# Optimization experiments

Measured on AMD Instinct MI355X. Metric: run time of the kernel, lower is better.

The kernel has to match this reference:

```python
import jax, jax.numpy as jnp
import numpy as np

N_NODES = 50000
N_EDGES = 800000
IN_FEAT = 128
NUM_CLASSES = 40


def _glorot(key, shape):
    fan_in, fan_out = shape
    lim = jnp.sqrt(6.0 / (fan_in + fan_out))
    return jax.random.uniform(key, shape, jnp.float32, -lim, lim)


def setup_inputs() -> dict:
    key = jax.random.key(0)
    ks = jax.random.split(key, 16)
    inp = {
        "x": jax.random.normal(ks[0], (N_NODES, IN_FEAT), jnp.float32),
        "edge_index": jax.random.randint(ks[1], (2, N_EDGES), 0, N_NODES, jnp.int64),
        "edge_weight": jax.random.uniform(ks[2], (N_EDGES,), jnp.float32),
        # GCNConv weights (PyG GCNConv: linear w/o bias, separate bias added after aggregation)
        "W1": _glorot(ks[3], (IN_FEAT, 512)), "b1": jnp.zeros((512,), jnp.float32),
        "W2": _glorot(ks[4], (512, 256)), "b2": jnp.zeros((256,), jnp.float32),
        "W3": _glorot(ks[5], (256, 128)), "b3": jnp.zeros((128,), jnp.float32),
        # MLP head
        "L1w": _glorot(ks[6], (128, 64)), "L1b": jnp.zeros((64,), jnp.float32),
        "L2w": _glorot(ks[7], (64, 32)), "L2b": jnp.zeros((32,), jnp.float32),
        "L3w": _glorot(ks[8], (32, NUM_CLASSES)), "L3b": jnp.zeros((NUM_CLASSES,), jnp.float32),
    }
    return inp


def _gcn_conv(x, W, b, src, dst, ew, n):
    # PyG GCNConv: add self-loops (weight 1), symmetric normalization D^-1/2 (A+I) D^-1/2,
    # linear transform first, then scatter-add aggregation, then bias.
    xw = x @ W  # [N, C_out]
    deg = jax.ops.segment_sum(ew, dst, num_segments=n) + 1.0  # +1 for self-loop weight
    dinv = jnp.where(deg > 0, jax.lax.rsqrt(deg), 0.0)  # [N]
    norm = dinv[src] * ew * dinv[dst]  # [E]
    out = jax.ops.segment_sum(norm[:, None] * xw[src], dst, num_segments=n)
    out = out + (dinv * dinv)[:, None] * xw  # self-loop contribution
    return out + b


def reference(x, edge_index, edge_weight, W1, b1, W2, b2, W3, b3,
              L1w, L1b, L2w, L2b, L3w, L3b):
    n = x.shape[0]
    src, dst = edge_index[0], edge_index[1]
    # conv stack; dropout p=0.0 -> identity (omitted)
    h = jax.nn.relu(_gcn_conv(x, W1, b1, src, dst, edge_weight, n))
    h = jax.nn.relu(_gcn_conv(h, W2, b2, src, dst, edge_weight, n))
    h = jax.nn.relu(_gcn_conv(h, W3, b3, src, dst, edge_weight, n))
    # MLP head
    h = jax.nn.relu(h @ L1w + L1b)
    h = jax.nn.relu(h @ L2w + L2b)
    h = h @ L3w + L3b
    return jax.nn.softmax(h, axis=1)
```

## Files before the change

### kernel.cpp

```cpp
#include <hip/hip_runtime.h>
#include <hip/hip_bf16.h>

#define N_NODES 50000
#define N_EDGES 800000
#define M_PAD 50048

typedef __attribute__((ext_vector_type(8))) short short8;
typedef __attribute__((ext_vector_type(4))) float float4_;

#define GLOAD_LDS(g, l) __builtin_amdgcn_global_load_lds( \
    (const __attribute__((address_space(1))) void*)(g),   \
    (__attribute__((address_space(3))) void*)(l), 16, 0, 0)

__device__ __forceinline__ unsigned short f2bf(float f) {
    unsigned int u = __float_as_uint(f);
    unsigned int r = (u + 0x7FFFu + ((u >> 16) & 1u)) >> 16;
    return (unsigned short)r;
}
__device__ __forceinline__ float bf2f(unsigned short h) {
    return __uint_as_float(((unsigned int)h) << 16);
}


__global__ __launch_bounds__(256) void deg_kernel(const int* __restrict__ dst,
                                                  const float* __restrict__ ew,
                                                  float* __restrict__ deg, int E) {
    int e = blockIdx.x * blockDim.x + threadIdx.x;
    if (e < E) atomicAdd(&deg[dst[e]], ew[e]);
}

__global__ __launch_bounds__(256) void dinv_kernel(float* __restrict__ deg, int n) {
    int i = blockIdx.x * blockDim.x + threadIdx.x;
    if (i < n) deg[i] = rsqrtf(deg[i] + 1.0f);
}


__global__ __launch_bounds__(256) void count_kernel(const int* __restrict__ dst,
                                                    int* __restrict__ cnt, int E) {
    int e = blockIdx.x * blockDim.x + threadIdx.x;
    if (e < E) atomicAdd(&cnt[dst[e]], 1);
}

__global__ __launch_bounds__(512) void scan_block_kernel(const int* __restrict__ cnt,
                                                         int* __restrict__ rowptr,
                                                         int* __restrict__ bsums, int n) {
    __shared__ int s[512];
    int t = threadIdx.x;
    int i = blockIdx.x * 512 + t;
    s[t] = (i < n) ? cnt[i] : 0;
    __syncthreads();
    for (int off = 1; off < 512; off <<= 1) {
        int v = (t >= off) ? s[t - off] : 0;
        __syncthreads();
        s[t] += v;
        __syncthreads();
    }
    if (i < n) rowptr[i + 1] = s[t];
    if (t == 511) bsums[blockIdx.x] = s[511];
}

__global__ void scan_sums_kernel(int* bsums, int nb) {
    if (threadIdx.x == 0 && blockIdx.x == 0) {
        int run = 0;
        for (int i = 0; i < nb; ++i) { int v = bsums[i]; bsums[i] = run; run += v; }
    }
}

__global__ __launch_bounds__(512) void scan_add_kernel(int* __restrict__ rowptr,
                                                       const int* __restrict__ bsums, int n) {
    int i = blockIdx.x * 512 + threadIdx.x;
    if (i < n) rowptr[i + 1] += bsums[blockIdx.x];
    if (i == 0) rowptr[0] = 0;
}

__global__ __launch_bounds__(256) void fill_kernel(const int* __restrict__ src,
                                                   const int* __restrict__ dst,
                                                   const float* __restrict__ ew,
                                                   const float* __restrict__ dinv,
                                                   int* __restrict__ cursor,
                                                   int* __restrict__ col,
                                                   float* __restrict__ val, int E) {
    int e = blockIdx.x * blockDim.x + threadIdx.x;
    if (e >= E) return;
    int d = dst[e];
    int s = src[e];
    int pos = atomicAdd(&cursor[d], 1);
    col[pos] = s;
    val[pos] = dinv[s] * ew[e];
}


__global__ __launch_bounds__(256) void wsplit_kernel(const float* __restrict__ Wm,
                                                     unsigned short* __restrict__ Th,
                                                     unsigned short* __restrict__ Tl,
                                                     int K, int N) {
    int idx = blockIdx.x * blockDim.x + threadIdx.x;
    if (idx >= K * N) return;
    int n = idx / K, k = idx - n * K;
    float v = Wm[(size_t)k * N + n];
    unsigned short hi = f2bf(v);
    float res = v - bf2f(hi);
    Th[idx] = hi;
    Tl[idx] = f2bf(res);
}


template <int C, bool BIAS, bool RELU, bool SPLIT>
__global__ __launch_bounds__(256) void gather_kernel(const float* __restrict__ t,
                                                     const int* __restrict__ rowptr,
                                                     const int* __restrict__ col,
                                                     const float* __restrict__ val,
                                                     const float* __restrict__ dinv,
                                                     const float* __restrict__ bias,
                                                     float* __restrict__ outf,
                                                     unsigned short* __restrict__ oh,
                                                     unsigned short* __restrict__ ol, int n) {
    constexpr int L = C / 4;
    constexpr int EPS = 64 / L;
    constexpr int U = 4;
    int wave = threadIdx.x >> 6, lane = threadIdx.x & 63;
    int slot = lane / L, li = lane % L;

    for (int node = blockIdx.x * 4 + wave; node < n; node += gridDim.x * 4) {
        int p0 = rowptr[node], p1 = rowptr[node + 1];
        float4 acc = {0.f, 0.f, 0.f, 0.f};
        for (int pb = p0; pb < p1; pb += U * EPS) {
            float a[U];
            float4 v[U];
#pragma unroll
            for (int u = 0; u < U; ++u) {
                int pe = pb + u * EPS + slot;
                int pec = min(pe, p1 - 1);
                int s = col[pec];
                float av = val[pec];
                a[u] = (pe < p1) ? av : 0.f;
                v[u] = *(const float4*)(t + (size_t)s * C + li * 4);
            }
#pragma unroll
            for (int u = 0; u < U; ++u) {
                acc.x += a[u] * v[u].x;
                acc.y += a[u] * v[u].y;
                acc.z += a[u] * v[u].z;
                acc.w += a[u] * v[u].w;
            }
        }
        if (EPS == 2) {
            acc.x += __shfl_xor(acc.x, 32);
            acc.y += __shfl_xor(acc.y, 32);
            acc.z += __shfl_xor(acc.z, 32);
            acc.w += __shfl_xor(acc.w, 32);
        }
        if (EPS == 1 || slot == 0) {
            float di = dinv[node];
            float s2 = di * di;
            float4 tv = *(const float4*)(t + (size_t)node * C + li * 4);
            float4 r;
            r.x = di * acc.x + s2 * tv.x;
            r.y = di * acc.y + s2 * tv.y;
            r.z = di * acc.z + s2 * tv.z;
            r.w = di * acc.w + s2 * tv.w;
            if (BIAS) {
                float4 b4 = *(const float4*)(bias + li * 4);
                r.x += b4.x; r.y += b4.y; r.z += b4.z; r.w += b4.w;
            }
            if (RELU) {
                r.x = fmaxf(r.x, 0.f); r.y = fmaxf(r.y, 0.f);
                r.z = fmaxf(r.z, 0.f); r.w = fmaxf(r.w, 0.f);
            }
            size_t base = (size_t)node * C + li * 4;
            if (SPLIT) {
                ushort4 h4, l4;
                float rv[4] = {r.x, r.y, r.z, r.w};
                unsigned short hs[4], lsx[4];
#pragma unroll
                for (int j = 0; j < 4; ++j) {
                    unsigned short hi = f2bf(rv[j]);
                    hs[j] = hi;
                    lsx[j] = f2bf(rv[j] - bf2f(hi));
                }
                h4.x = hs[0]; h4.y = hs[1]; h4.z = hs[2]; h4.w = hs[3];
                l4.x = lsx[0]; l4.y = lsx[1]; l4.z = lsx[2]; l4.w = lsx[3];
                *(ushort4*)(oh + base) = h4;
                *(ushort4*)(ol + base) = l4;
            } else {
                *(float4*)(outf + base) = r;
            }
        }
    }
}


template <int OUTMODE>
__global__ __launch_bounds__(256, 2) void mfma_gemm(const unsigned short* __restrict__ Ah,
                                                    const unsigned short* __restrict__ Al,
                                                    const unsigned short* __restrict__ Bh,
                                                    const unsigned short* __restrict__ Bl,
                                                    const float* __restrict__ bias,
                                                    float* __restrict__ Cf,
                                                    unsigned short* __restrict__ Ch,
                                                    unsigned short* __restrict__ Cl,
                                                    int K, int N) {
    __shared__ unsigned short sAh[128 * 64];
    __shared__ unsigned short sAl[128 * 64];
    __shared__ unsigned short sBh[128 * 64];
    __shared__ unsigned short sBl[128 * 64];

    int tid = threadIdx.x;
    int lane = tid & 63, w = tid >> 6;
    int m0 = blockIdx.x * 128, n0 = blockIdx.y * 128;

    const unsigned short* gsrc = (w == 0) ? Ah : (w == 1) ? Al : (w == 2) ? Bh : Bl;
    unsigned short* sbase = (w == 0) ? sAh : (w == 1) ? sAl : (w == 2) ? sBh : sBl;
    int grow0 = ((w < 2) ? m0 : n0) + (lane >> 3);
    int gcol = ((lane & 7) ^ ((lane >> 3) & 7)) * 8;
    const unsigned short* gptr0 = gsrc + (size_t)grow0 * K + gcol;

    float4_ acc[4][4] = {};

    int wm = (w >> 1) * 64, wn = (w & 1) * 64;
    int lr = lane & 15, lg = lane >> 4;

    for (int k0 = 0; k0 < K; k0 += 64) {
        const unsigned short* gp = gptr0 + k0;
#pragma unroll
        for (int q = 0; q < 16; ++q)
            GLOAD_LDS(gp + (size_t)(8 * q) * K, sbase + q * 512);
        __syncthreads();

#pragma unroll
        for (int ks = 0; ks < 2; ++ks) {
            short8 ahf[4], alf[4], bhf[4], blf[4];
#pragma unroll
            for (int f = 0; f < 4; ++f) {
                int ra = wm + f * 16 + lr;
                int sa = (((ks << 2) | lg) ^ (ra & 7)) * 16;
                ahf[f] = *(const short8*)((const char*)sAh + ra * 128 + sa);
                alf[f] = *(const short8*)((const char*)sAl + ra * 128 + sa);
                int rb = wn + f * 16 + lr;
                int sb = (((ks << 2) | lg) ^ (rb & 7)) * 16;
                bhf[f] = *(const short8*)((const char*)sBh + rb * 128 + sb);
                blf[f] = *(const short8*)((const char*)sBl + rb * 128 + sb);
            }
#pragma unroll
            for (int i = 0; i < 4; ++i)
#pragma unroll
                for (int j = 0; j < 4; ++j) {
                    acc[i][j] = __builtin_amdgcn_mfma_f32_16x16x32_bf16(ahf[i], bhf[j], acc[i][j], 0, 0, 0);
                    acc[i][j] = __builtin_amdgcn_mfma_f32_16x16x32_bf16(ahf[i], blf[j], acc[i][j], 0, 0, 0);
                    acc[i][j] = __builtin_amdgcn_mfma_f32_16x16x32_bf16(alf[i], bhf[j], acc[i][j], 0, 0, 0);
                }
        }
        __syncthreads();
    }

#pragma unroll
    for (int i = 0; i < 4; ++i) {
        int row0 = m0 + wm + i * 16 + lg * 4;
#pragma unroll
        for (int j = 0; j < 4; ++j) {
            int colg = n0 + wn + j * 16 + lr;
            float b = (OUTMODE == 1) ? bias[colg] : 0.f;
#pragma unroll
            for (int r = 0; r < 4; ++r) {
                float v = acc[i][j][r] + b;
                size_t idx = (size_t)(row0 + r) * N + colg;
                if (OUTMODE == 1) {
                    v = fmaxf(v, 0.f);
                    unsigned short hi = f2bf(v);
                    float res = v - bf2f(hi);
                    Ch[idx] = hi;
                    Cl[idx] = f2bf(res);
                } else {
                    Cf[idx] = v;
                }
            }
        }
    }
}


__global__ __launch_bounds__(256) void mlp_kernel(const float* __restrict__ h,
                                                  const float* __restrict__ W1, const float* __restrict__ b1,
                                                  const float* __restrict__ W2, const float* __restrict__ b2,
                                                  const float* __restrict__ W3, const float* __restrict__ b3,
                                                  float* __restrict__ out, int n) {
    __shared__ float W1s[128 * 64];
    __shared__ float W2s[64 * 32];
    __shared__ float W3s[32 * 40];
    __shared__ float b1s[64], b2s[32], b3s[40];
    __shared__ float hs[4][128];
    __shared__ float h1s[4][64];
    __shared__ float h2s[4][32];
    __shared__ float ls[4][40];
    __shared__ float es[4][40];

    int tid = threadIdx.x;
    for (int i = tid; i < 128 * 64; i += 256) W1s[i] = W1[i];
    for (int i = tid; i < 64 * 32; i += 256) W2s[i] = W2[i];
    for (int i = tid; i < 32 * 40; i += 256) W3s[i] = W3[i];
    if (tid < 64) b1s[tid] = b1[tid];
    if (tid < 32) b2s[tid] = b2[tid];
    if (tid < 40) b3s[tid] = b3[tid];
    __syncthreads();

    int wave = tid >> 6, lane = tid & 63;

    for (int base = blockIdx.x * 4; base < n; base += gridDim.x * 4) {
        int node = base + wave;
        if (node < n) {
            hs[wave][lane]      = fmaxf(h[(size_t)node * 128 + lane], 0.f);
            hs[wave][lane + 64] = fmaxf(h[(size_t)node * 128 + lane + 64], 0.f);
        }
        __syncthreads();
        {
            float acc = b1s[lane];
#pragma unroll 8
            for (int k = 0; k < 128; ++k) acc += hs[wave][k] * W1s[k * 64 + lane];
            h1s[wave][lane] = fmaxf(acc, 0.f);
        }
        __syncthreads();
        if (lane < 32) {
            float acc = b2s[lane];
#pragma unroll 8
            for (int k = 0; k < 64; ++k) acc += h1s[wave][k] * W2s[k * 32 + lane];
            h2s[wave][lane] = fmaxf(acc, 0.f);
        }
        __syncthreads();
        if (lane < 40) {
            float acc = b3s[lane];
#pragma unroll 8
            for (int k = 0; k < 32; ++k) acc += h2s[wave][k] * W3s[k * 40 + lane];
            ls[wave][lane] = acc;
        }
        __syncthreads();
        float e = 0.f;
        if (lane < 40) {
            float m = -1e30f;
            for (int j = 0; j < 40; ++j) m = fmaxf(m, ls[wave][j]);
            e = expf(ls[wave][lane] - m);
            es[wave][lane] = e;
        }
        __syncthreads();
        if (node < n && lane < 40) {
            float s = 0.f;
            for (int j = 0; j < 40; ++j) s += es[wave][j];
            out[(size_t)node * 40 + lane] = e / s;
        }
        __syncthreads();
    }
}


extern "C" void kernel_launch(void* const* d_in, const int* in_sizes, int n_in,
                              void* d_out, int out_size, void* d_ws, size_t ws_size,
                              hipStream_t stream) {
    const float* x   = (const float*)d_in[0];
    const int*   ei  = (const int*)d_in[1];
    const float* ew  = (const float*)d_in[2];
    const float* W1  = (const float*)d_in[3];
    const float* b1  = (const float*)d_in[4];
    const float* W2  = (const float*)d_in[5];
    const float* b2  = (const float*)d_in[6];
    const float* W3  = (const float*)d_in[7];
    const float* b3  = (const float*)d_in[8];
    const float* L1w = (const float*)d_in[9];
    const float* L1b = (const float*)d_in[10];
    const float* L2w = (const float*)d_in[11];
    const float* L2b = (const float*)d_in[12];
    const float* L3w = (const float*)d_in[13];
    const float* L3b = (const float*)d_in[14];
    float* out = (float*)d_out;

    const int n = N_NODES, E = N_EDGES;
    const int* src = ei;
    const int* dst = ei + E;

    char* wsb = (char*)d_ws;
    size_t off = 0;
    auto alloc = [&](size_t bytes) -> char* {
        char* p = wsb + off;
        off += (bytes + 255) & ~(size_t)255;
        return p;
    };
    float* dinv   = (float*)alloc(N_NODES * 4);
    int* rowptr   = (int*)alloc((N_NODES + 1) * 4);
    int* cursor   = (int*)alloc(N_NODES * 4);
    int* colb     = (int*)alloc((size_t)N_EDGES * 4);
    float* val    = (float*)alloc((size_t)N_EDGES * 4);
    int* bsums    = (int*)alloc(256 * 4);
    unsigned short* W1th = (unsigned short*)alloc(512 * 128 * 2);
    unsigned short* W1tl = (unsigned short*)alloc(512 * 128 * 2);
    unsigned short* W2th = (unsigned short*)alloc(256 * 512 * 2);
    unsigned short* W2tl = (unsigned short*)alloc(256 * 512 * 2);
    unsigned short* W3th = (unsigned short*)alloc(128 * 256 * 2);
    unsigned short* W3tl = (unsigned short*)alloc(128 * 256 * 2);
    unsigned short* aggXh = (unsigned short*)alloc((size_t)M_PAD * 128 * 2);
    unsigned short* aggXl = (unsigned short*)alloc((size_t)M_PAD * 128 * 2);
    unsigned short* h1h  = (unsigned short*)alloc((size_t)M_PAD * 512 * 2);
    unsigned short* h1l  = (unsigned short*)alloc((size_t)M_PAD * 512 * 2);
    float* t2     = (float*)alloc((size_t)M_PAD * 256 * 4);
    unsigned short* agg2h = aggXh;
    unsigned short* agg2l = (unsigned short*)h1h;
    float* t3   = (float*)((char*)h1h + (size_t)M_PAD * 256 * 2);
    float* agg3 = (float*)h1l;

    const int nb = (n + 511) / 512;

    hipMemsetAsync(dinv, 0, n * sizeof(float), stream);
    deg_kernel<<<(E + 255) / 256, 256, 0, stream>>>(dst, ew, dinv, E);
    dinv_kernel<<<(n + 255) / 256, 256, 0, stream>>>(dinv, n);

    wsplit_kernel<<<(128 * 512 + 255) / 256, 256, 0, stream>>>(W1, W1th, W1tl, 128, 512);
    wsplit_kernel<<<(512 * 256 + 255) / 256, 256, 0, stream>>>(W2, W2th, W2tl, 512, 256);
    wsplit_kernel<<<(256 * 128 + 255) / 256, 256, 0, stream>>>(W3, W3th, W3tl, 256, 128);

    hipMemsetAsync(cursor, 0, n * sizeof(int), stream);
    count_kernel<<<(E + 255) / 256, 256, 0, stream>>>(dst, cursor, E);
    scan_block_kernel<<<nb, 512, 0, stream>>>(cursor, rowptr, bsums, n);
    scan_sums_kernel<<<1, 64, 0, stream>>>(bsums, nb);
    scan_add_kernel<<<nb, 512, 0, stream>>>(rowptr, bsums, n);
    hipMemcpyAsync(cursor, rowptr, n * sizeof(int), hipMemcpyDeviceToDevice, stream);
    fill_kernel<<<(E + 255) / 256, 256, 0, stream>>>(src, dst, ew, dinv, cursor, colb, val, E);

    gather_kernel<128, false, false, true><<<(n + 3) / 4, 256, 0, stream>>>(
        x, rowptr, colb, val, dinv, nullptr, nullptr, aggXh, aggXl, n);
    {
        dim3 g(M_PAD / 128, 512 / 128);
        mfma_gemm<1><<<g, 256, 0, stream>>>(aggXh, aggXl, W1th, W1tl, b1, nullptr, h1h, h1l, 128, 512);
    }
    {
        dim3 g(M_PAD / 128, 256 / 128);
        mfma_gemm<0><<<g, 256, 0, stream>>>(h1h, h1l, W2th, W2tl, nullptr, t2, nullptr, nullptr, 512, 256);
    }
    gather_kernel<256, true, true, true><<<(n + 3) / 4, 256, 0, stream>>>(
        t2, rowptr, colb, val, dinv, b2, nullptr, agg2h, agg2l, n);
    {
        dim3 g(M_PAD / 128, 128 / 128);
        mfma_gemm<0><<<g, 256, 0, stream>>>(agg2h, agg2l, W3th, W3tl, nullptr, t3, nullptr, nullptr, 256, 128);
    }
    gather_kernel<128, true, false, false><<<(n + 3) / 4, 256, 0, stream>>>(
        t3, rowptr, colb, val, dinv, b3, agg3, nullptr, nullptr, n);
    mlp_kernel<<<1024, 256, 0, stream>>>(agg3, L1w, L1b, L2w, L2b, L3w, L3b, out, n);
}
```

Measured before the change: 715.4 us.

## Shard gather kernels by feature column slices and fuse degree/count atomics

The SpMM gather kernels are restructured so each block handles one of eight column slices for four nodes. The point is to keep the working set of gathered feature rows per slice small enough to stay cache-resident, and to spread each node's edges across more lanes with a cross-lane reduction at the end. In exchange, col/val index reads are repeated eight times and each gathered access is narrower. The degree and in-degree count atomics are also merged into one pass over dst.

```diff
diff --git a/kernel.cpp b/kernel.cpp
--- a/kernel.cpp
+++ b/kernel.cpp
@@ -22,11 +22,16 @@
 }
 
 
-__global__ __launch_bounds__(256) void deg_kernel(const int* __restrict__ dst,
-                                                  const float* __restrict__ ew,
-                                                  float* __restrict__ deg, int E) {
+__global__ __launch_bounds__(256) void degcnt_kernel(const int* __restrict__ dst,
+                                                     const float* __restrict__ ew,
+                                                     float* __restrict__ deg,
+                                                     int* __restrict__ cnt, int E) {
     int e = blockIdx.x * blockDim.x + threadIdx.x;
-    if (e < E) atomicAdd(&deg[dst[e]], ew[e]);
+    if (e < E) {
+        int d = dst[e];
+        atomicAdd(&deg[d], ew[e]);
+        atomicAdd(&cnt[d], 1);
+    }
 }
 
 __global__ __launch_bounds__(256) void dinv_kernel(float* __restrict__ deg, int n) {
@@ -34,12 +39,6 @@
     if (i < n) deg[i] = rsqrtf(deg[i] + 1.0f);
 }
 
-
-__global__ __launch_bounds__(256) void count_kernel(const int* __restrict__ dst,
-                                                    int* __restrict__ cnt, int E) {
-    int e = blockIdx.x * blockDim.x + threadIdx.x;
-    if (e < E) atomicAdd(&cnt[dst[e]], 1);
-}
 
 __global__ __launch_bounds__(512) void scan_block_kernel(const int* __restrict__ cnt,
                                                          int* __restrict__ rowptr,
@@ -106,85 +105,92 @@
 
 
 template <int C, bool BIAS, bool RELU, bool SPLIT>
-__global__ __launch_bounds__(256) void gather_kernel(const float* __restrict__ t,
-                                                     const int* __restrict__ rowptr,
-                                                     const int* __restrict__ col,
-                                                     const float* __restrict__ val,
-                                                     const float* __restrict__ dinv,
-                                                     const float* __restrict__ bias,
-                                                     float* __restrict__ outf,
-                                                     unsigned short* __restrict__ oh,
-                                                     unsigned short* __restrict__ ol, int n) {
-    constexpr int L = C / 4;
-    constexpr int EPS = 64 / L;
-    constexpr int U = 4;
+__global__ __launch_bounds__(256) void gather_shard(const float* __restrict__ t,
+                                                    const int* __restrict__ rowptr,
+                                                    const int* __restrict__ col,
+                                                    const float* __restrict__ val,
+                                                    const float* __restrict__ dinv,
+                                                    const float* __restrict__ bias,
+                                                    float* __restrict__ outf,
+                                                    unsigned short* __restrict__ oh,
+                                                    unsigned short* __restrict__ ol, int n) {
+    constexpr int SC = C / 8;
+    constexpr int LPE = SC / 4;
+    constexpr int EPW = 64 / LPE;
+    constexpr int U = 2;
+    int slice = blockIdx.x & 7;
+    int nodeblk = blockIdx.x >> 3;
     int wave = threadIdx.x >> 6, lane = threadIdx.x & 63;
-    int slot = lane / L, li = lane % L;
-
-    for (int node = blockIdx.x * 4 + wave; node < n; node += gridDim.x * 4) {
-        int p0 = rowptr[node], p1 = rowptr[node + 1];
-        float4 acc = {0.f, 0.f, 0.f, 0.f};
-        for (int pb = p0; pb < p1; pb += U * EPS) {
-            float a[U];
-            float4 v[U];
-#pragma unroll
-            for (int u = 0; u < U; ++u) {
-                int pe = pb + u * EPS + slot;
-                int pec = min(pe, p1 - 1);
-                int s = col[pec];
-                float av = val[pec];
-                a[u] = (pe < p1) ? av : 0.f;
-                v[u] = *(const float4*)(t + (size_t)s * C + li * 4);
+    int slot = lane / LPE;
+    int li = lane % LPE;
+    int colofs = slice * SC + li * 4;
+
+    int node = nodeblk * 4 + wave;
+    if (node >= n) return;
+
+    int p0 = rowptr[node], p1 = rowptr[node + 1];
+    float4 acc = {0.f, 0.f, 0.f, 0.f};
+    for (int pb = p0; pb < p1; pb += U * EPW) {
+        float a[U];
+        float4 v[U];
+#pragma unroll
+        for (int u = 0; u < U; ++u) {
+            int pe = pb + u * EPW + slot;
+            int pec = min(pe, p1 - 1);
+            int s = col[pec];
+            float av = val[pec];
+            a[u] = (pe < p1) ? av : 0.f;
+            v[u] = *(const float4*)(t + (size_t)s * C + colofs);
+        }
+#pragma unroll
+        for (int u = 0; u < U; ++u) {
+            acc.x += a[u] * v[u].x;
+            acc.y += a[u] * v[u].y;
+            acc.z += a[u] * v[u].z;
+            acc.w += a[u] * v[u].w;
+        }
+    }
+#pragma unroll
+    for (int m = LPE; m <= 32; m <<= 1) {
+        acc.x += __shfl_xor(acc.x, m);
+        acc.y += __shfl_xor(acc.y, m);
+        acc.z += __shfl_xor(acc.z, m);
+        acc.w += __shfl_xor(acc.w, m);
+    }
+    if (slot == 0) {
+        float di = dinv[node];
+        float s2 = di * di;
+        float4 tv = *(const float4*)(t + (size_t)node * C + colofs);
+        float4 r;
+        r.x = di * acc.x + s2 * tv.x;
+        r.y = di * acc.y + s2 * tv.y;
+        r.z = di * acc.z + s2 * tv.z;
+        r.w = di * acc.w + s2 * tv.w;
+        if (BIAS) {
+            float4 b4 = *(const float4*)(bias + colofs);
+            r.x += b4.x; r.y += b4.y; r.z += b4.z; r.w += b4.w;
+        }
+        if (RELU) {
+            r.x = fmaxf(r.x, 0.f); r.y = fmaxf(r.y, 0.f);
+            r.z = fmaxf(r.z, 0.f); r.w = fmaxf(r.w, 0.f);
+        }
+        size_t base = (size_t)node * C + colofs;
+        if (SPLIT) {
+            float rv[4] = {r.x, r.y, r.z, r.w};
+            ushort4 h4, l4;
+            unsigned short hs[4], lsx[4];
+#pragma unroll
+            for (int j = 0; j < 4; ++j) {
+                unsigned short hi = f2bf(rv[j]);
+                hs[j] = hi;
+                lsx[j] = f2bf(rv[j] - bf2f(hi));
             }
-#pragma unroll
-            for (int u = 0; u < U; ++u) {
-                acc.x += a[u] * v[u].x;
-                acc.y += a[u] * v[u].y;
-                acc.z += a[u] * v[u].z;
-                acc.w += a[u] * v[u].w;
-            }
-        }
-        if (EPS == 2) {
-            acc.x += __shfl_xor(acc.x, 32);
-            acc.y += __shfl_xor(acc.y, 32);
-            acc.z += __shfl_xor(acc.z, 32);
-            acc.w += __shfl_xor(acc.w, 32);
-        }
-        if (EPS == 1 || slot == 0) {
-            float di = dinv[node];
-            float s2 = di * di;
-            float4 tv = *(const float4*)(t + (size_t)node * C + li * 4);
-            float4 r;
-            r.x = di * acc.x + s2 * tv.x;
-            r.y = di * acc.y + s2 * tv.y;
-            r.z = di * acc.z + s2 * tv.z;
-            r.w = di * acc.w + s2 * tv.w;
-            if (BIAS) {
-                float4 b4 = *(const float4*)(bias + li * 4);
-                r.x += b4.x; r.y += b4.y; r.z += b4.z; r.w += b4.w;
-            }
-            if (RELU) {
-                r.x = fmaxf(r.x, 0.f); r.y = fmaxf(r.y, 0.f);
-                r.z = fmaxf(r.z, 0.f); r.w = fmaxf(r.w, 0.f);
-            }
-            size_t base = (size_t)node * C + li * 4;
-            if (SPLIT) {
-                ushort4 h4, l4;
-                float rv[4] = {r.x, r.y, r.z, r.w};
-                unsigned short hs[4], lsx[4];
-#pragma unroll
-                for (int j = 0; j < 4; ++j) {
-                    unsigned short hi = f2bf(rv[j]);
-                    hs[j] = hi;
-                    lsx[j] = f2bf(rv[j] - bf2f(hi));
-                }
-                h4.x = hs[0]; h4.y = hs[1]; h4.z = hs[2]; h4.w = hs[3];
-                l4.x = lsx[0]; l4.y = lsx[1]; l4.z = lsx[2]; l4.w = lsx[3];
-                *(ushort4*)(oh + base) = h4;
-                *(ushort4*)(ol + base) = l4;
-            } else {
-                *(float4*)(outf + base) = r;
-            }
+            h4.x = hs[0]; h4.y = hs[1]; h4.z = hs[2]; h4.w = hs[3];
+            l4.x = lsx[0]; l4.y = lsx[1]; l4.z = lsx[2]; l4.w = lsx[3];
+            *(ushort4*)(oh + base) = h4;
+            *(ushort4*)(ol + base) = l4;
+        } else {
+            *(float4*)(outf + base) = r;
         }
     }
 }
@@ -405,24 +411,24 @@
     float* agg3 = (float*)h1l;
 
     const int nb = (n + 511) / 512;
+    const int gshard = ((n + 3) / 4) * 8;
 
     hipMemsetAsync(dinv, 0, n * sizeof(float), stream);
-    deg_kernel<<<(E + 255) / 256, 256, 0, stream>>>(dst, ew, dinv, E);
+    hipMemsetAsync(cursor, 0, n * sizeof(int), stream);
+    degcnt_kernel<<<(E + 255) / 256, 256, 0, stream>>>(dst, ew, dinv, cursor, E);
     dinv_kernel<<<(n + 255) / 256, 256, 0, stream>>>(dinv, n);
 
     wsplit_kernel<<<(128 * 512 + 255) / 256, 256, 0, stream>>>(W1, W1th, W1tl, 128, 512);
     wsplit_kernel<<<(512 * 256 + 255) / 256, 256, 0, stream>>>(W2, W2th, W2tl, 512, 256);
     wsplit_kernel<<<(256 * 128 + 255) / 256, 256, 0, stream>>>(W3, W3th, W3tl, 256, 128);
 
-    hipMemsetAsync(cursor, 0, n * sizeof(int), stream);
-    count_kernel<<<(E + 255) / 256, 256, 0, stream>>>(dst, cursor, E);
     scan_block_kernel<<<nb, 512, 0, stream>>>(cursor, rowptr, bsums, n);
     scan_sums_kernel<<<1, 64, 0, stream>>>(bsums, nb);
     scan_add_kernel<<<nb, 512, 0, stream>>>(rowptr, bsums, n);
     hipMemcpyAsync(cursor, rowptr, n * sizeof(int), hipMemcpyDeviceToDevice, stream);
     fill_kernel<<<(E + 255) / 256, 256, 0, stream>>>(src, dst, ew, dinv, cursor, colb, val, E);
 
-    gather_kernel<128, false, false, true><<<(n + 3) / 4, 256, 0, stream>>>(
+    gather_shard<128, false, false, true><<<gshard, 256, 0, stream>>>(
         x, rowptr, colb, val, dinv, nullptr, nullptr, aggXh, aggXl, n);
     {
         dim3 g(M_PAD / 128, 512 / 128);
@@ -432,13 +438,13 @@
         dim3 g(M_PAD / 128, 256 / 128);
         mfma_gemm<0><<<g, 256, 0, stream>>>(h1h, h1l, W2th, W2tl, nullptr, t2, nullptr, nullptr, 512, 256);
     }
-    gather_kernel<256, true, true, true><<<(n + 3) / 4, 256, 0, stream>>>(
+    gather_shard<256, true, true, true><<<gshard, 256, 0, stream>>>(
         t2, rowptr, colb, val, dinv, b2, nullptr, agg2h, agg2l, n);
     {
         dim3 g(M_PAD / 128, 128 / 128);
         mfma_gemm<0><<<g, 256, 0, stream>>>(agg2h, agg2l, W3th, W3tl, nullptr, t3, nullptr, nullptr, 256, 128);
     }
-    gather_kernel<128, true, false, false><<<(n + 3) / 4, 256, 0, stream>>>(
+    gather_shard<128, true, false, false><<<gshard, 256, 0, stream>>>(
         t3, rowptr, colb, val, dinv, b3, agg3, nullptr, nullptr, n);
     mlp_kernel<<<1024, 256, 0, stream>>>(agg3, L1w, L1b, L2w, L2b, L3w, L3b, out, n);
 }
```

After: 870.5 us. 21.7% more time.
